# Optimization experiments

Hardware: AMD Instinct MI355X
Metric: run time of the kernel (lower is better)

## Reference

```python
import jax, jax.numpy as jnp
import numpy as np

EMBED_SIZE = 1024
HEADS = 16
HEAD_DIM = EMBED_SIZE // HEADS
N, L = 2, 2048


def setup_inputs() -> dict:
    key = jax.random.key(0)
    ks = jax.random.split(key, 6)
    values = jax.random.normal(ks[0], (N, L, EMBED_SIZE), dtype=jnp.float32)
    keys_t = jax.random.normal(ks[1], (N, L, EMBED_SIZE), dtype=jnp.float32)
    query = jax.random.normal(ks[2], (N, L, EMBED_SIZE), dtype=jnp.float32)
    mask = jax.random.randint(ks[3], (N, 1, L, L), 0, 2, dtype=jnp.int32)
    # fc_out params (torch Linear: y = x @ W.T + b)
    Wo = jax.random.normal(ks[4], (EMBED_SIZE, EMBED_SIZE), dtype=jnp.float32) * (EMBED_SIZE ** -0.5)
    bo = jax.random.normal(ks[5], (EMBED_SIZE,), dtype=jnp.float32) * 0.01
    return {"values": values, "keys": keys_t, "query": query, "mask": mask, "Wo": Wo, "bo": bo}


def reference(values, keys, query, mask, Wo, bo):
    # NOTE: the original torch module defines per-head q/k/v Linears but never
    # calls them in forward; only fc_out is applied. We reproduce that exactly.
    n, q_len, _ = query.shape
    v = values.reshape(n, -1, HEADS, HEAD_DIM)   # nkhd
    k = keys.reshape(n, -1, HEADS, HEAD_DIM)     # nkhd
    q = query.reshape(n, q_len, HEADS, HEAD_DIM) # nqhd
    energy = jnp.einsum('nqhd,nkhd->nhqk', q, k)
    energy = jnp.where(mask == 0, jnp.float32(-1e20), energy)
    scale = jnp.float32(EMBED_SIZE) ** 0.5  # sqrt(embed_size), as in source
    attn = jax.nn.softmax(energy / scale, axis=3)
    out = jnp.einsum('nhqk,nkhd->nqhd', attn, v).reshape(n, q_len, HEADS * HEAD_DIM)
    return out @ Wo.T + bo
```

## Files before the change

### kernel.cpp

```cpp
#include <hip/hip_runtime.h>
#include <hip/hip_bf16.h>
#include <stdint.h>

#define LSEQ 2048
#define NBATCH 2
#define NHEADS 16
#define HDIM 64
#define EMB 1024

typedef __bf16 bf16x8 __attribute__((ext_vector_type(8)));
typedef float f32x4 __attribute__((ext_vector_type(4)));
typedef unsigned short ushort4v __attribute__((ext_vector_type(4)));
typedef unsigned short ushort8v __attribute__((ext_vector_type(8)));

#define QSCALE (1.44269504088896f / 32.0f)

static __device__ __forceinline__ unsigned short f2bf(float f) {
  union { float f; uint32_t u; } v; v.f = f;
  uint32_t u = v.u;
  u += 0x7fffu + ((u >> 16) & 1u);
  return (unsigned short)(u >> 16);
}

static __device__ __forceinline__ f32x4 mfma16(bf16x8 a, bf16x8 b, f32x4 c) {
  return __builtin_amdgcn_mfma_f32_16x16x32_bf16(a, b, c, 0, 0, 0);
}

static __device__ __forceinline__ float mexp2(float e, uint32_t m, int b) {
  uint32_t keep = (uint32_t)__builtin_amdgcn_sbfe((int)m, b, 1);
  return __uint_as_float(__float_as_uint(__builtin_amdgcn_exp2f(e)) & keep);
}

__global__ __launch_bounds__(256) void prep_kernel(
    const float* __restrict__ q, const float* __restrict__ k,
    const float* __restrict__ w, const int* __restrict__ mask,
    const float* __restrict__ v,
    unsigned short* __restrict__ qb, unsigned short* __restrict__ kb,
    unsigned short* __restrict__ wb, unsigned char* __restrict__ mb8,
    unsigned short* __restrict__ vt) {
  int b = blockIdx.x;
  if (b < 8192) {
    int idx = b * 256 + threadIdx.x;
    const float* src; unsigned short* dst; int t; int swz;
    if (idx < (1 << 20)) { src = q; dst = qb; t = idx; swz = 0; }
    else                 { src = k; dst = kb; t = idx - (1 << 20); swz = 1; }
    int e = t << 2;
    int d = e & 63;
    int h = (e >> 6) & 15;
    int l = (e >> 10) & (LSEQ - 1);
    int n = e >> 21;
    float4 vv = reinterpret_cast<const float4*>(src)[t];
    int dd = d;
    if (swz) dd = ((((d >> 3) ^ (l & 7)) << 3) | (d & 7));
    else { vv.x *= QSCALE; vv.y *= QSCALE; vv.z *= QSCALE; vv.w *= QSCALE; }
    ushort4v o;
    o.x = f2bf(vv.x); o.y = f2bf(vv.y); o.z = f2bf(vv.z); o.w = f2bf(vv.w);
    size_t oi = (((size_t)n * NHEADS + h) * LSEQ + l) * HDIM + dd;
    *reinterpret_cast<ushort4v*>(dst + oi) = o;
  } else if (b < 9216) {
    int t = (b - 8192) * 256 + threadIdx.x;
    float4 vv = reinterpret_cast<const float4*>(w)[t];
    ushort4v o;
    o.x = f2bf(vv.x); o.y = f2bf(vv.y); o.z = f2bf(vv.z); o.w = f2bf(vv.w);
    reinterpret_cast<ushort4v*>(wb)[t] = o;
  } else if (b < 13312) {
    int idx = (b - 9216) * 256 + threadIdx.x;
    const int* mp = mask + (size_t)idx * 8;
    int4 m0 = *reinterpret_cast<const int4*>(mp);
    int4 m1 = *reinterpret_cast<const int4*>(mp + 4);
    unsigned int bb = (m0.x ? 1u : 0u) | (m0.y ? 2u : 0u) | (m0.z ? 4u : 0u) |
                      (m0.w ? 8u : 0u) | (m1.x ? 16u : 0u) | (m1.y ? 32u : 0u) |
                      (m1.z ? 64u : 0u) | (m1.w ? 128u : 0u);
    mb8[idx] = (unsigned char)bb;
  } else {
    int b2 = b - 13312;
    int kc = b2 & 63;
    int h  = (b2 >> 6) & 15;
    int n  = b2 >> 10;
    int t  = threadIdx.x;
    int d    = t & 63;
    int sgrp = t >> 6;
    const float* src = v + (size_t)n * LSEQ * EMB + h * HDIM + d;
    ushort8v o;
#pragma unroll
    for (int j = 0; j < 8; ++j) {
      int kp = (j < 4) ? (4 * sgrp + j) : (16 + 4 * sgrp + (j - 4));
      float f = src[(size_t)(kc * 32 + kp) * EMB];
      o[j] = f2bf(f);
    }
    int cs = sgrp ^ ((d >> 1) & 3);
    size_t base = (((size_t)(n * NHEADS + h) * 64 + kc) * HDIM + d) * 32 + (cs << 3);
    *reinterpret_cast<ushort8v*>(vt + base) = o;
  }
}

__global__ __launch_bounds__(256, 4) void attn_kernel(
    const unsigned short* __restrict__ Kb, const unsigned short* __restrict__ Qb,
    const unsigned short* __restrict__ VT, const uint32_t* __restrict__ maskw,
    unsigned short* __restrict__ Op) {
  __shared__ unsigned short lds[2][8192];

  int bid = blockIdx.x;
  bid = (bid & 7) * 128 + (bid >> 3);
  int qt = bid & 31;
  int h  = (bid >> 5) & 15;
  int n  = bid >> 9;
  int tid  = threadIdx.x;
  int wave = tid >> 6;
  int lane = tid & 63;
  int g  = lane >> 4;
  int qi = lane & 15;
  int qrow = qt * 64 + wave * 16 + qi;

  const unsigned short* qptr = Qb + (((size_t)n * NHEADS + h) * LSEQ + qrow) * HDIM;
  bf16x8 bq0 = *reinterpret_cast<const bf16x8*>(qptr + g * 8);
  bf16x8 bq1 = *reinterpret_cast<const bf16x8*>(qptr + 32 + g * 8);

  const unsigned short* khead  = Kb + (((size_t)n * NHEADS + h) * LSEQ) * HDIM;
  const unsigned short* vthead = VT + ((size_t)(n * NHEADS + h) * 64) * (HDIM * 32);
  const uint32_t* mrow = maskw + ((size_t)n * LSEQ + qrow) * 64;

  int xk = qi & 7;
  int kA = qi * 64 + ((g ^ xk) << 3);
  int kB = qi * 64 + (((4 + g) ^ xk) << 3);
  int kC = kA + 1024;
  int kD = kB + 1024;
  int xv = (qi >> 1) & 3;
  int vA = qi * 32 + ((g ^ xv) << 3);
  int vB = vA + 512;
  int vC = vA + 1024;
  int vD = vA + 1536;

  f32x4 z = {0.f, 0.f, 0.f, 0.f};
  f32x4 acc0 = z, acc1 = z, acc2 = z, acc3 = z;
  float ssum = 0.f;

#define STAGE(T, BUF) do {                                                     \
    const unsigned short* kg_ = khead  + (size_t)(T) * 4096 + tid * 8;         \
    const unsigned short* vg_ = vthead + (size_t)(T) * 4096 + tid * 8;         \
    __builtin_amdgcn_global_load_lds(                                          \
        (const __attribute__((address_space(1))) uint32_t*)kg_,                \
        (__attribute__((address_space(3))) uint32_t*)&lds[BUF][wave * 512],    \
        16, 0, 0);                                                             \
    __builtin_amdgcn_global_load_lds(                                          \
        (const __attribute__((address_space(1))) uint32_t*)(kg_ + 2048),       \
        (__attribute__((address_space(3))) uint32_t*)&lds[BUF][2048 + wave * 512], \
        16, 0, 0);                                                             \
    __builtin_amdgcn_global_load_lds(                                          \
        (const __attribute__((address_space(1))) uint32_t*)vg_,                \
        (__attribute__((address_space(3))) uint32_t*)&lds[BUF][4096 + wave * 512], \
        16, 0, 0);                                                             \
    __builtin_amdgcn_global_load_lds(                                          \
        (const __attribute__((address_space(1))) uint32_t*)(vg_ + 2048),       \
        (__attribute__((address_space(3))) uint32_t*)&lds[BUF][6144 + wave * 512], \
        16, 0, 0);                                                             \
  } while (0)

#define COMPUTE(BUF, CH, MW) do {                                              \
    const unsigned short* lk_ = &lds[BUF][(CH) * 2048];                        \
    const unsigned short* lv_ = &lds[BUF][4096 + (CH) * 2048];                 \
    bf16x8 K0 = *(const bf16x8*)(lk_ + kA);                                    \
    bf16x8 K1 = *(const bf16x8*)(lk_ + kB);                                    \
    bf16x8 K2 = *(const bf16x8*)(lk_ + kC);                                    \
    bf16x8 K3 = *(const bf16x8*)(lk_ + kD);                                    \
    f32x4 e0 = z, e1 = z;                                                      \
    e0 = mfma16(K0, bq0, e0); e0 = mfma16(K1, bq1, e0);                        \
    e1 = mfma16(K2, bq0, e1); e1 = mfma16(K3, bq1, e1);                        \
    uint32_t m0_ = (MW) >> (4 * g);                                            \
    uint32_t m1_ = (MW) >> (16 + 4 * g);                                       \
    float p0 = mexp2(e0[0], m0_, 0);                                           \
    float p1 = mexp2(e0[1], m0_, 1);                                           \
    float p2 = mexp2(e0[2], m0_, 2);                                           \
    float p3 = mexp2(e0[3], m0_, 3);                                           \
    float p4 = mexp2(e1[0], m1_, 0);                                           \
    float p5 = mexp2(e1[1], m1_, 1);                                           \
    float p6 = mexp2(e1[2], m1_, 2);                                           \
    float p7 = mexp2(e1[3], m1_, 3);                                           \
    ssum += ((p0 + p1) + (p2 + p3)) + ((p4 + p5) + (p6 + p7));                 \
    union { uint32_t u[4]; bf16x8 v; } pf;                                     \
    asm("v_cvt_pk_bf16_f32 %0, %1, %2" : "=v"(pf.u[0]) : "v"(p0), "v"(p1));    \
    asm("v_cvt_pk_bf16_f32 %0, %1, %2" : "=v"(pf.u[1]) : "v"(p2), "v"(p3));    \
    asm("v_cvt_pk_bf16_f32 %0, %1, %2" : "=v"(pf.u[2]) : "v"(p4), "v"(p5));    \
    asm("v_cvt_pk_bf16_f32 %0, %1, %2" : "=v"(pf.u[3]) : "v"(p6), "v"(p7));    \
    bf16x8 V0 = *(const bf16x8*)(lv_ + vA);                                    \
    bf16x8 V1 = *(const bf16x8*)(lv_ + vB);                                    \
    bf16x8 V2 = *(const bf16x8*)(lv_ + vC);                                    \
    bf16x8 V3 = *(const bf16x8*)(lv_ + vD);                                    \
    acc0 = mfma16(V0, pf.v, acc0);                                             \
    acc1 = mfma16(V1, pf.v, acc1);                                             \
    acc2 = mfma16(V2, pf.v, acc2);                                             \
    acc3 = mfma16(V3, pf.v, acc3);                                             \
  } while (0)

  uint64_t mp0 = *(const uint64_t*)(mrow);
  uint64_t mp1, mp2;
  STAGE(0, 0);
  __syncthreads();

  for (int t = 0; t < 32; t += 2) {
    int t1 = (t + 1) & 31;
    mp1 = *(const uint64_t*)(mrow + 2 * t1);
    STAGE(t1, 1);
    COMPUTE(0, 0, (uint32_t)mp0);
    COMPUTE(0, 1, (uint32_t)(mp0 >> 32));
    __syncthreads();
    int t2 = (t + 2) & 31;
    mp2 = *(const uint64_t*)(mrow + 2 * t2);
    STAGE(t2, 0);
    COMPUTE(1, 0, (uint32_t)mp1);
    COMPUTE(1, 1, (uint32_t)(mp1 >> 32));
    __syncthreads();
    mp0 = mp2;
  }
#undef STAGE
#undef COMPUTE

  ssum += __shfl_xor(ssum, 16, 64);
  ssum += __shfl_xor(ssum, 32, 64);
  float inv = 1.0f / ssum;

  size_t ob = ((size_t)n * LSEQ + qrow) * EMB + h * HDIM;
  ushort4v s0, s1, s2, s3;
#pragma unroll
  for (int r = 0; r < 4; ++r) {
    s0[r] = f2bf(acc0[r] * inv);
    s1[r] = f2bf(acc1[r] * inv);
    s2[r] = f2bf(acc2[r] * inv);
    s3[r] = f2bf(acc3[r] * inv);
  }
  *reinterpret_cast<ushort4v*>(Op + ob + 0  + 4 * g) = s0;
  *reinterpret_cast<ushort4v*>(Op + ob + 16 + 4 * g) = s1;
  *reinterpret_cast<ushort4v*>(Op + ob + 32 + 4 * g) = s2;
  *reinterpret_cast<ushort4v*>(Op + ob + 48 + 4 * g) = s3;
}

__global__ __launch_bounds__(256, 2) void proj_kernel(
    const unsigned short* __restrict__ A, const unsigned short* __restrict__ B,
    const float* __restrict__ bo, float* __restrict__ out) {
  __shared__ unsigned short plds[2][6144];

  int bid = blockIdx.x;
  bid = (bid & 7) * 64 + (bid >> 3);
  int mb0 = (bid >> 4) * 128;
  int nb0 = (bid & 15) * 64;
  int tid  = threadIdx.x;
  int wave = tid >> 6;
  int lane = tid & 63;
  int g  = lane >> 4;
  int qi = lane & 15;
  int wm = wave >> 1, wn = wave & 1;

  int srow = tid >> 2;
  int scol = (((tid & 3) ^ ((tid >> 3) & 3)) << 3);
  const unsigned short* aS0 = A + (size_t)(mb0 + srow) * EMB + scol;
  const unsigned short* aS1 = aS0 + (size_t)64 * EMB;
  const unsigned short* bS  = B + (size_t)(nb0 + srow) * EMB + scol;

  int xa = (qi >> 1) & 3;
  int gof = ((g ^ xa) << 3);
  int aof0 = (wm * 64 + qi) * 32 + gof;
  int aof1 = aof0 + 16 * 32;
  int aof2 = aof0 + 32 * 32;
  int aof3 = aof0 + 48 * 32;
  int bof0 = (wn * 32 + qi) * 32 + gof;
  int bof1 = bof0 + 16 * 32;

  f32x4 z = {0.f, 0.f, 0.f, 0.f};
  f32x4 acc00 = z, acc01 = z, acc10 = z, acc11 = z;
  f32x4 acc20 = z, acc21 = z, acc30 = z, acc31 = z;

#define PSTAGE(KT, BUF) do {                                                   \
    __builtin_amdgcn_global_load_lds(                                          \
        (const __attribute__((address_space(1))) uint32_t*)(aS0 + (KT) * 32),  \
        (__attribute__((address_space(3))) uint32_t*)&plds[BUF][wave * 512],   \
        16, 0, 0);                                                             \
    __builtin_amdgcn_global_load_lds(                                          \
        (const __attribute__((address_space(1))) uint32_t*)(aS1 + (KT) * 32),  \
        (__attribute__((address_space(3))) uint32_t*)&plds[BUF][2048 + wave * 512], \
        16, 0, 0);                                                             \
    __builtin_amdgcn_global_load_lds(                                          \
        (const __attribute__((address_space(1))) uint32_t*)(bS + (KT) * 32),   \
        (__attribute__((address_space(3))) uint32_t*)&plds[BUF][4096 + wave * 512], \
        16, 0, 0);                                                             \
  } while (0)

#define PCOMPUTE(BUF) do {                                                     \
    const unsigned short* la_ = &plds[BUF][0];                                 \
    const unsigned short* lb_ = &plds[BUF][4096];                              \
    bf16x8 a0 = *(const bf16x8*)(la_ + aof0);                                  \
    bf16x8 a1 = *(const bf16x8*)(la_ + aof1);                                  \
    bf16x8 a2 = *(const bf16x8*)(la_ + aof2);                                  \
    bf16x8 a3 = *(const bf16x8*)(la_ + aof3);                                  \
    bf16x8 b0 = *(const bf16x8*)(lb_ + bof0);                                  \
    bf16x8 b1 = *(const bf16x8*)(lb_ + bof1);                                  \
    acc00 = mfma16(a0, b0, acc00); acc01 = mfma16(a0, b1, acc01);              \
    acc10 = mfma16(a1, b0, acc10); acc11 = mfma16(a1, b1, acc11);              \
    acc20 = mfma16(a2, b0, acc20); acc21 = mfma16(a2, b1, acc21);              \
    acc30 = mfma16(a3, b0, acc30); acc31 = mfma16(a3, b1, acc31);              \
  } while (0)

  PSTAGE(0, 0);
  __syncthreads();
  for (int kt = 0; kt < 32; kt += 2) {
    PSTAGE(kt + 1, 1);
    PCOMPUTE(0);
    __syncthreads();
    PSTAGE((kt + 2) & 31, 0);
    PCOMPUTE(1);
    __syncthreads();
  }
#undef PSTAGE
#undef PCOMPUTE

  int orow = mb0 + wm * 64 + 4 * g;
  int col0 = nb0 + wn * 32 + qi;
  float bia0 = bo[col0];
  float bia1 = bo[col0 + 16];
#define PSTORE(ACC0, ACC1, M) do {                                             \
    _Pragma("unroll")                                                          \
    for (int r = 0; r < 4; ++r) {                                              \
      size_t rw = (size_t)(orow + (M) * 16 + r) * EMB;                         \
      out[rw + col0]      = ACC0[r] + bia0;                                    \
      out[rw + col0 + 16] = ACC1[r] + bia1;                                    \
    }                                                                          \
  } while (0)
  PSTORE(acc00, acc01, 0);
  PSTORE(acc10, acc11, 1);
  PSTORE(acc20, acc21, 2);
  PSTORE(acc30, acc31, 3);
#undef PSTORE
}

extern "C" void kernel_launch(void* const* d_in, const int* in_sizes, int n_in,
                              void* d_out, int out_size, void* d_ws, size_t ws_size,
                              hipStream_t stream) {
  const float* Vf   = (const float*)d_in[0];
  const float* Kf   = (const float*)d_in[1];
  const float* Qf   = (const float*)d_in[2];
  const int*   Mask = (const int*)d_in[3];
  const float* Wo   = (const float*)d_in[4];
  const float* Bo   = (const float*)d_in[5];
  float* out = (float*)d_out;

  char* ws = (char*)d_ws;
  unsigned short* Qb  = (unsigned short*)(ws);
  unsigned short* Kb  = (unsigned short*)(ws + (size_t)8  * 1024 * 1024);
  unsigned short* VTb = (unsigned short*)(ws + (size_t)16 * 1024 * 1024);
  unsigned short* Wob = (unsigned short*)(ws + (size_t)24 * 1024 * 1024);
  unsigned short* Opb = (unsigned short*)(ws + (size_t)26 * 1024 * 1024);
  unsigned char*  Mb  = (unsigned char*)(ws + (size_t)34 * 1024 * 1024);

  prep_kernel<<<15360, 256, 0, stream>>>(Qf, Kf, Wo, Mask, Vf, Qb, Kb, Wob, Mb, VTb);
  attn_kernel<<<1024, 256, 0, stream>>>(Kb, Qb, VTb, (const uint32_t*)Mb, Opb);
  proj_kernel<<<512, 256, 0, stream>>>(Opb, Wob, Bo, out);
}
```

Before: 90.59 us.

## Process two 16-row query tiles per wave to reuse K/V LDS tiles

Each attention block now covers 128 query rows instead of 64, with each wave handling two 16-row query groups that share the same K and V fragments loaded from LDS. This halves the global-to-LDS K/V staging traffic per query and the number of blocks (1024 to 512). In exchange it doubles the accumulator registers, lowers the occupancy hint to 2 blocks per CU, and 512 blocks may underfill the 256 CUs relative to before.

```diff
diff --git a/kernel.cpp b/kernel.cpp
--- a/kernel.cpp
+++ b/kernel.cpp
@@ -94,31 +94,34 @@
   }
 }
 
-__global__ __launch_bounds__(256, 4) void attn_kernel(
+__global__ __launch_bounds__(256, 2) void attn_kernel(
     const unsigned short* __restrict__ Kb, const unsigned short* __restrict__ Qb,
     const unsigned short* __restrict__ VT, const uint32_t* __restrict__ maskw,
     unsigned short* __restrict__ Op) {
   __shared__ unsigned short lds[2][8192];
 
   int bid = blockIdx.x;
-  bid = (bid & 7) * 128 + (bid >> 3);
-  int qt = bid & 31;
-  int h  = (bid >> 5) & 15;
-  int n  = bid >> 9;
+  bid = (bid & 7) * 64 + (bid >> 3);
+  int qt = bid & 15;
+  int h  = (bid >> 4) & 15;
+  int n  = bid >> 8;
   int tid  = threadIdx.x;
   int wave = tid >> 6;
   int lane = tid & 63;
   int g  = lane >> 4;
   int qi = lane & 15;
-  int qrow = qt * 64 + wave * 16 + qi;
+  int qrow = qt * 128 + wave * 16 + qi;
 
   const unsigned short* qptr = Qb + (((size_t)n * NHEADS + h) * LSEQ + qrow) * HDIM;
   bf16x8 bq0 = *reinterpret_cast<const bf16x8*>(qptr + g * 8);
   bf16x8 bq1 = *reinterpret_cast<const bf16x8*>(qptr + 32 + g * 8);
+  bf16x8 bq2 = *reinterpret_cast<const bf16x8*>(qptr + 64 * HDIM + g * 8);
+  bf16x8 bq3 = *reinterpret_cast<const bf16x8*>(qptr + 64 * HDIM + 32 + g * 8);
 
   const unsigned short* khead  = Kb + (((size_t)n * NHEADS + h) * LSEQ) * HDIM;
   const unsigned short* vthead = VT + ((size_t)(n * NHEADS + h) * 64) * (HDIM * 32);
-  const uint32_t* mrow = maskw + ((size_t)n * LSEQ + qrow) * 64;
+  const uint32_t* mrow0 = maskw + ((size_t)n * LSEQ + qrow) * 64;
+  const uint32_t* mrow1 = mrow0 + 64 * 64;
 
   int xk = qi & 7;
   int kA = qi * 64 + ((g ^ xk) << 3);
@@ -133,7 +136,8 @@
 
   f32x4 z = {0.f, 0.f, 0.f, 0.f};
   f32x4 acc0 = z, acc1 = z, acc2 = z, acc3 = z;
-  float ssum = 0.f;
+  f32x4 acc4 = z, acc5 = z, acc6 = z, acc7 = z;
+  float ssum0 = 0.f, ssum1 = 0.f;
 
 #define STAGE(T, BUF) do {                                                     \
     const unsigned short* kg_ = khead  + (size_t)(T) * 4096 + tid * 8;         \
@@ -156,82 +160,123 @@
         16, 0, 0);                                                             \
   } while (0)
 
-#define COMPUTE(BUF, CH, MW) do {                                              \
+#define COMPUTE(BUF, CH, MA, MB) do {                                          \
     const unsigned short* lk_ = &lds[BUF][(CH) * 2048];                        \
     const unsigned short* lv_ = &lds[BUF][4096 + (CH) * 2048];                 \
     bf16x8 K0 = *(const bf16x8*)(lk_ + kA);                                    \
     bf16x8 K1 = *(const bf16x8*)(lk_ + kB);                                    \
     bf16x8 K2 = *(const bf16x8*)(lk_ + kC);                                    \
     bf16x8 K3 = *(const bf16x8*)(lk_ + kD);                                    \
-    f32x4 e0 = z, e1 = z;                                                      \
+    f32x4 e0 = z, e1 = z, f0 = z, f1 = z;                                      \
     e0 = mfma16(K0, bq0, e0); e0 = mfma16(K1, bq1, e0);                        \
     e1 = mfma16(K2, bq0, e1); e1 = mfma16(K3, bq1, e1);                        \
-    uint32_t m0_ = (MW) >> (4 * g);                                            \
-    uint32_t m1_ = (MW) >> (16 + 4 * g);                                       \
-    float p0 = mexp2(e0[0], m0_, 0);                                           \
-    float p1 = mexp2(e0[1], m0_, 1);                                           \
-    float p2 = mexp2(e0[2], m0_, 2);                                           \
-    float p3 = mexp2(e0[3], m0_, 3);                                           \
-    float p4 = mexp2(e1[0], m1_, 0);                                           \
-    float p5 = mexp2(e1[1], m1_, 1);                                           \
-    float p6 = mexp2(e1[2], m1_, 2);                                           \
-    float p7 = mexp2(e1[3], m1_, 3);                                           \
-    ssum += ((p0 + p1) + (p2 + p3)) + ((p4 + p5) + (p6 + p7));                 \
-    union { uint32_t u[4]; bf16x8 v; } pf;                                     \
-    asm("v_cvt_pk_bf16_f32 %0, %1, %2" : "=v"(pf.u[0]) : "v"(p0), "v"(p1));    \
-    asm("v_cvt_pk_bf16_f32 %0, %1, %2" : "=v"(pf.u[1]) : "v"(p2), "v"(p3));    \
-    asm("v_cvt_pk_bf16_f32 %0, %1, %2" : "=v"(pf.u[2]) : "v"(p4), "v"(p5));    \
-    asm("v_cvt_pk_bf16_f32 %0, %1, %2" : "=v"(pf.u[3]) : "v"(p6), "v"(p7));    \
+    f0 = mfma16(K0, bq2, f0); f0 = mfma16(K1, bq3, f0);                        \
+    f1 = mfma16(K2, bq2, f1); f1 = mfma16(K3, bq3, f1);                        \
     bf16x8 V0 = *(const bf16x8*)(lv_ + vA);                                    \
     bf16x8 V1 = *(const bf16x8*)(lv_ + vB);                                    \
     bf16x8 V2 = *(const bf16x8*)(lv_ + vC);                                    \
     bf16x8 V3 = *(const bf16x8*)(lv_ + vD);                                    \
-    acc0 = mfma16(V0, pf.v, acc0);                                             \
-    acc1 = mfma16(V1, pf.v, acc1);                                             \
-    acc2 = mfma16(V2, pf.v, acc2);                                             \
-    acc3 = mfma16(V3, pf.v, acc3);                                             \
+    {                                                                          \
+      uint32_t m0_ = (MA) >> (4 * g);                                          \
+      uint32_t m1_ = (MA) >> (16 + 4 * g);                                     \
+      float p0 = mexp2(e0[0], m0_, 0);                                         \
+      float p1 = mexp2(e0[1], m0_, 1);                                         \
+      float p2 = mexp2(e0[2], m0_, 2);                                         \
+      float p3 = mexp2(e0[3], m0_, 3);                                         \
+      float p4 = mexp2(e1[0], m1_, 0);                                         \
+      float p5 = mexp2(e1[1], m1_, 1);                                         \
+      float p6 = mexp2(e1[2], m1_, 2);                                         \
+      float p7 = mexp2(e1[3], m1_, 3);                                         \
+      ssum0 += ((p0 + p1) + (p2 + p3)) + ((p4 + p5) + (p6 + p7));              \
+      union { uint32_t u[4]; bf16x8 v; } pf;                                   \
+      asm("v_cvt_pk_bf16_f32 %0, %1, %2" : "=v"(pf.u[0]) : "v"(p0), "v"(p1));  \
+      asm("v_cvt_pk_bf16_f32 %0, %1, %2" : "=v"(pf.u[1]) : "v"(p2), "v"(p3));  \
+      asm("v_cvt_pk_bf16_f32 %0, %1, %2" : "=v"(pf.u[2]) : "v"(p4), "v"(p5));  \
+      asm("v_cvt_pk_bf16_f32 %0, %1, %2" : "=v"(pf.u[3]) : "v"(p6), "v"(p7));  \
+      acc0 = mfma16(V0, pf.v, acc0);                                           \
+      acc1 = mfma16(V1, pf.v, acc1);                                           \
+      acc2 = mfma16(V2, pf.v, acc2);                                           \
+      acc3 = mfma16(V3, pf.v, acc3);                                           \
+    }                                                                          \
+    {                                                                          \
+      uint32_t m0_ = (MB) >> (4 * g);                                          \
+      uint32_t m1_ = (MB) >> (16 + 4 * g);                                     \
+      float r0 = mexp2(f0[0], m0_, 0);                                         \
+      float r1 = mexp2(f0[1], m0_, 1);                                         \
+      float r2 = mexp2(f0[2], m0_, 2);                                         \
+      float r3 = mexp2(f0[3], m0_, 3);                                         \
+      float r4 = mexp2(f1[0], m1_, 0);                                         \
+      float r5 = mexp2(f1[1], m1_, 1);                                         \
+      float r6 = mexp2(f1[2], m1_, 2);                                         \
+      float r7 = mexp2(f1[3], m1_, 3);                                         \
+      ssum1 += ((r0 + r1) + (r2 + r3)) + ((r4 + r5) + (r6 + r7));              \
+      union { uint32_t u[4]; bf16x8 v; } pg;                                   \
+      asm("v_cvt_pk_bf16_f32 %0, %1, %2" : "=v"(pg.u[0]) : "v"(r0), "v"(r1));  \
+      asm("v_cvt_pk_bf16_f32 %0, %1, %2" : "=v"(pg.u[1]) : "v"(r2), "v"(r3));  \
+      asm("v_cvt_pk_bf16_f32 %0, %1, %2" : "=v"(pg.u[2]) : "v"(r4), "v"(r5));  \
+      asm("v_cvt_pk_bf16_f32 %0, %1, %2" : "=v"(pg.u[3]) : "v"(r6), "v"(r7));  \
+      acc4 = mfma16(V0, pg.v, acc4);                                           \
+      acc5 = mfma16(V1, pg.v, acc5);                                           \
+      acc6 = mfma16(V2, pg.v, acc6);                                           \
+      acc7 = mfma16(V3, pg.v, acc7);                                           \
+    }                                                                          \
   } while (0)
 
-  uint64_t mp0 = *(const uint64_t*)(mrow);
-  uint64_t mp1, mp2;
+  uint64_t ma0 = *(const uint64_t*)(mrow0);
+  uint64_t mb0 = *(const uint64_t*)(mrow1);
+  uint64_t ma1, mb1, ma2, mb2;
   STAGE(0, 0);
   __syncthreads();
 
   for (int t = 0; t < 32; t += 2) {
     int t1 = (t + 1) & 31;
-    mp1 = *(const uint64_t*)(mrow + 2 * t1);
+    ma1 = *(const uint64_t*)(mrow0 + 2 * t1);
+    mb1 = *(const uint64_t*)(mrow1 + 2 * t1);
     STAGE(t1, 1);
-    COMPUTE(0, 0, (uint32_t)mp0);
-    COMPUTE(0, 1, (uint32_t)(mp0 >> 32));
+    COMPUTE(0, 0, (uint32_t)ma0, (uint32_t)mb0);
+    COMPUTE(0, 1, (uint32_t)(ma0 >> 32), (uint32_t)(mb0 >> 32));
     __syncthreads();
     int t2 = (t + 2) & 31;
-    mp2 = *(const uint64_t*)(mrow + 2 * t2);
+    ma2 = *(const uint64_t*)(mrow0 + 2 * t2);
+    mb2 = *(const uint64_t*)(mrow1 + 2 * t2);
     STAGE(t2, 0);
-    COMPUTE(1, 0, (uint32_t)mp1);
-    COMPUTE(1, 1, (uint32_t)(mp1 >> 32));
+    COMPUTE(1, 0, (uint32_t)ma1, (uint32_t)mb1);
+    COMPUTE(1, 1, (uint32_t)(ma1 >> 32), (uint32_t)(mb1 >> 32));
     __syncthreads();
-    mp0 = mp2;
+    ma0 = ma2; mb0 = mb2;
   }
 #undef STAGE
 #undef COMPUTE
 
-  ssum += __shfl_xor(ssum, 16, 64);
-  ssum += __shfl_xor(ssum, 32, 64);
-  float inv = 1.0f / ssum;
-
-  size_t ob = ((size_t)n * LSEQ + qrow) * EMB + h * HDIM;
-  ushort4v s0, s1, s2, s3;
+  ssum0 += __shfl_xor(ssum0, 16, 64);
+  ssum0 += __shfl_xor(ssum0, 32, 64);
+  ssum1 += __shfl_xor(ssum1, 16, 64);
+  ssum1 += __shfl_xor(ssum1, 32, 64);
+  float inv0 = 1.0f / ssum0;
+  float inv1 = 1.0f / ssum1;
+
+  size_t ob0 = ((size_t)n * LSEQ + qrow) * EMB + h * HDIM;
+  size_t ob1 = ob0 + (size_t)64 * EMB;
+  ushort4v s0, s1, s2, s3, s4, s5, s6, s7;
 #pragma unroll
   for (int r = 0; r < 4; ++r) {
-    s0[r] = f2bf(acc0[r] * inv);
-    s1[r] = f2bf(acc1[r] * inv);
-    s2[r] = f2bf(acc2[r] * inv);
-    s3[r] = f2bf(acc3[r] * inv);
+    s0[r] = f2bf(acc0[r] * inv0);
+    s1[r] = f2bf(acc1[r] * inv0);
+    s2[r] = f2bf(acc2[r] * inv0);
+    s3[r] = f2bf(acc3[r] * inv0);
+    s4[r] = f2bf(acc4[r] * inv1);
+    s5[r] = f2bf(acc5[r] * inv1);
+    s6[r] = f2bf(acc6[r] * inv1);
+    s7[r] = f2bf(acc7[r] * inv1);
   }
-  *reinterpret_cast<ushort4v*>(Op + ob + 0  + 4 * g) = s0;
-  *reinterpret_cast<ushort4v*>(Op + ob + 16 + 4 * g) = s1;
-  *reinterpret_cast<ushort4v*>(Op + ob + 32 + 4 * g) = s2;
-  *reinterpret_cast<ushort4v*>(Op + ob + 48 + 4 * g) = s3;
+  *reinterpret_cast<ushort4v*>(Op + ob0 + 0  + 4 * g) = s0;
+  *reinterpret_cast<ushort4v*>(Op + ob0 + 16 + 4 * g) = s1;
+  *reinterpret_cast<ushort4v*>(Op + ob0 + 32 + 4 * g) = s2;
+  *reinterpret_cast<ushort4v*>(Op + ob0 + 48 + 4 * g) = s3;
+  *reinterpret_cast<ushort4v*>(Op + ob1 + 0  + 4 * g) = s4;
+  *reinterpret_cast<ushort4v*>(Op + ob1 + 16 + 4 * g) = s5;
+  *reinterpret_cast<ushort4v*>(Op + ob1 + 32 + 4 * g) = s6;
+  *reinterpret_cast<ushort4v*>(Op + ob1 + 48 + 4 * g) = s7;
 }
 
 __global__ __launch_bounds__(256, 2) void proj_kernel(
@@ -351,6 +396,6 @@
   unsigned char*  Mb  = (unsigned char*)(ws + (size_t)34 * 1024 * 1024);
 
   prep_kernel<<<15360, 256, 0, stream>>>(Qf, Kf, Wo, Mask, Vf, Qb, Kb, Wob, Mb, VTb);
-  attn_kernel<<<1024, 256, 0, stream>>>(Kb, Qb, VTb, (const uint32_t*)Mb, Opb);
+  attn_kernel<<<512, 256, 0, stream>>>(Kb, Qb, VTb, (const uint32_t*)Mb, Opb);
   proj_kernel<<<512, 256, 0, stream>>>(Opb, Wob, Bo, out);
 }
```

After: 89.48 us. Within noise of the previous version (-1.2%).

## Stream K-only tiles through LDS, read V directly from global, MFMA row sums

Applied to the files above, without the earlier changes.

Only K tiles are staged in LDS now, each stage covering 128 keys instead of 64, with four compute chunks per stage. V fragments are read straight from global memory (L2/L1) in fragment-ready layout, so the V swizzle is dropped. The softmax denominator is accumulated with an extra MFMA against a ones vector instead of scalar adds and cross-lane shuffles. This halves the LDS/barrier count per key but puts V global-load latency on the critical path of each chunk.

```diff
diff --git a/kernel.cpp b/kernel.cpp
--- a/kernel.cpp
+++ b/kernel.cpp
@@ -88,8 +88,7 @@
       float f = src[(size_t)(kc * 32 + kp) * EMB];
       o[j] = f2bf(f);
     }
-    int cs = sgrp ^ ((d >> 1) & 3);
-    size_t base = (((size_t)(n * NHEADS + h) * 64 + kc) * HDIM + d) * 32 + (cs << 3);
+    size_t base = (((size_t)(n * NHEADS + h) * 64 + kc) * HDIM + d) * 32 + (sgrp << 3);
     *reinterpret_cast<ushort8v*>(vt + base) = o;
   }
 }
@@ -125,40 +124,31 @@
   int kB = qi * 64 + (((4 + g) ^ xk) << 3);
   int kC = kA + 1024;
   int kD = kB + 1024;
-  int xv = (qi >> 1) & 3;
-  int vA = qi * 32 + ((g ^ xv) << 3);
-  int vB = vA + 512;
-  int vC = vA + 1024;
-  int vD = vA + 1536;
+  int vA = qi * 32 + g * 8;
+
+  union { uint32_t u[4]; bf16x8 v; } ones;
+  ones.u[0] = 0x3F803F80u; ones.u[1] = 0x3F803F80u;
+  ones.u[2] = 0x3F803F80u; ones.u[3] = 0x3F803F80u;
 
   f32x4 z = {0.f, 0.f, 0.f, 0.f};
   f32x4 acc0 = z, acc1 = z, acc2 = z, acc3 = z;
-  float ssum = 0.f;
+  f32x4 sacc = z;
 
 #define STAGE(T, BUF) do {                                                     \
-    const unsigned short* kg_ = khead  + (size_t)(T) * 4096 + tid * 8;         \
-    const unsigned short* vg_ = vthead + (size_t)(T) * 4096 + tid * 8;         \
-    __builtin_amdgcn_global_load_lds(                                          \
-        (const __attribute__((address_space(1))) uint32_t*)kg_,                \
-        (__attribute__((address_space(3))) uint32_t*)&lds[BUF][wave * 512],    \
-        16, 0, 0);                                                             \
-    __builtin_amdgcn_global_load_lds(                                          \
-        (const __attribute__((address_space(1))) uint32_t*)(kg_ + 2048),       \
-        (__attribute__((address_space(3))) uint32_t*)&lds[BUF][2048 + wave * 512], \
-        16, 0, 0);                                                             \
-    __builtin_amdgcn_global_load_lds(                                          \
-        (const __attribute__((address_space(1))) uint32_t*)vg_,                \
-        (__attribute__((address_space(3))) uint32_t*)&lds[BUF][4096 + wave * 512], \
-        16, 0, 0);                                                             \
-    __builtin_amdgcn_global_load_lds(                                          \
-        (const __attribute__((address_space(1))) uint32_t*)(vg_ + 2048),       \
-        (__attribute__((address_space(3))) uint32_t*)&lds[BUF][6144 + wave * 512], \
-        16, 0, 0);                                                             \
-  } while (0)
-
-#define COMPUTE(BUF, CH, MW) do {                                              \
+    const unsigned short* kg_ = khead + (size_t)(T) * 8192 + tid * 8;          \
+    _Pragma("unroll")                                                          \
+    for (int j_ = 0; j_ < 4; ++j_) {                                           \
+      __builtin_amdgcn_global_load_lds(                                        \
+          (const __attribute__((address_space(1))) uint32_t*)(kg_ + j_ * 2048),\
+          (__attribute__((address_space(3))) uint32_t*)                        \
+              &lds[BUF][j_ * 2048 + wave * 512],                               \
+          16, 0, 0);                                                           \
+    }                                                                          \
+  } while (0)
+
+#define COMPUTE(BUF, CH, KC, MW) do {                                          \
     const unsigned short* lk_ = &lds[BUF][(CH) * 2048];                        \
-    const unsigned short* lv_ = &lds[BUF][4096 + (CH) * 2048];                 \
+    const unsigned short* vc_ = vthead + (size_t)(KC) * 2048;                  \
     bf16x8 K0 = *(const bf16x8*)(lk_ + kA);                                    \
     bf16x8 K1 = *(const bf16x8*)(lk_ + kB);                                    \
     bf16x8 K2 = *(const bf16x8*)(lk_ + kC);                                    \
@@ -166,6 +156,10 @@
     f32x4 e0 = z, e1 = z;                                                      \
     e0 = mfma16(K0, bq0, e0); e0 = mfma16(K1, bq1, e0);                        \
     e1 = mfma16(K2, bq0, e1); e1 = mfma16(K3, bq1, e1);                        \
+    bf16x8 V0 = *(const bf16x8*)(vc_ + vA);                                    \
+    bf16x8 V1 = *(const bf16x8*)(vc_ + vA + 512);                              \
+    bf16x8 V2 = *(const bf16x8*)(vc_ + vA + 1024);                             \
+    bf16x8 V3 = *(const bf16x8*)(vc_ + vA + 1536);                             \
     uint32_t m0_ = (MW) >> (4 * g);                                            \
     uint32_t m1_ = (MW) >> (16 + 4 * g);                                       \
     float p0 = mexp2(e0[0], m0_, 0);                                           \
@@ -176,48 +170,46 @@
     float p5 = mexp2(e1[1], m1_, 1);                                           \
     float p6 = mexp2(e1[2], m1_, 2);                                           \
     float p7 = mexp2(e1[3], m1_, 3);                                           \
-    ssum += ((p0 + p1) + (p2 + p3)) + ((p4 + p5) + (p6 + p7));                 \
     union { uint32_t u[4]; bf16x8 v; } pf;                                     \
     asm("v_cvt_pk_bf16_f32 %0, %1, %2" : "=v"(pf.u[0]) : "v"(p0), "v"(p1));    \
     asm("v_cvt_pk_bf16_f32 %0, %1, %2" : "=v"(pf.u[1]) : "v"(p2), "v"(p3));    \
     asm("v_cvt_pk_bf16_f32 %0, %1, %2" : "=v"(pf.u[2]) : "v"(p4), "v"(p5));    \
     asm("v_cvt_pk_bf16_f32 %0, %1, %2" : "=v"(pf.u[3]) : "v"(p6), "v"(p7));    \
-    bf16x8 V0 = *(const bf16x8*)(lv_ + vA);                                    \
-    bf16x8 V1 = *(const bf16x8*)(lv_ + vB);                                    \
-    bf16x8 V2 = *(const bf16x8*)(lv_ + vC);                                    \
-    bf16x8 V3 = *(const bf16x8*)(lv_ + vD);                                    \
     acc0 = mfma16(V0, pf.v, acc0);                                             \
     acc1 = mfma16(V1, pf.v, acc1);                                             \
     acc2 = mfma16(V2, pf.v, acc2);                                             \
     acc3 = mfma16(V3, pf.v, acc3);                                             \
-  } while (0)
-
-  uint64_t mp0 = *(const uint64_t*)(mrow);
-  uint64_t mp1, mp2;
+    sacc = mfma16(ones.v, pf.v, sacc);                                         \
+  } while (0)
+
+  uint4 mw0 = *(const uint4*)(mrow);
+  uint4 mw1, mw2;
   STAGE(0, 0);
   __syncthreads();
 
-  for (int t = 0; t < 32; t += 2) {
-    int t1 = (t + 1) & 31;
-    mp1 = *(const uint64_t*)(mrow + 2 * t1);
+  for (int t = 0; t < 16; t += 2) {
+    int t1 = (t + 1) & 15;
+    mw1 = *(const uint4*)(mrow + 4 * t1);
     STAGE(t1, 1);
-    COMPUTE(0, 0, (uint32_t)mp0);
-    COMPUTE(0, 1, (uint32_t)(mp0 >> 32));
+    COMPUTE(0, 0, t * 4 + 0, mw0.x);
+    COMPUTE(0, 1, t * 4 + 1, mw0.y);
+    COMPUTE(0, 2, t * 4 + 2, mw0.z);
+    COMPUTE(0, 3, t * 4 + 3, mw0.w);
     __syncthreads();
-    int t2 = (t + 2) & 31;
-    mp2 = *(const uint64_t*)(mrow + 2 * t2);
+    int t2 = (t + 2) & 15;
+    mw2 = *(const uint4*)(mrow + 4 * t2);
     STAGE(t2, 0);
-    COMPUTE(1, 0, (uint32_t)mp1);
-    COMPUTE(1, 1, (uint32_t)(mp1 >> 32));
+    COMPUTE(1, 0, t1 * 4 + 0, mw1.x);
+    COMPUTE(1, 1, t1 * 4 + 1, mw1.y);
+    COMPUTE(1, 2, t1 * 4 + 2, mw1.z);
+    COMPUTE(1, 3, t1 * 4 + 3, mw1.w);
     __syncthreads();
-    mp0 = mp2;
+    mw0 = mw2;
   }
 #undef STAGE
 #undef COMPUTE
 
-  ssum += __shfl_xor(ssum, 16, 64);
-  ssum += __shfl_xor(ssum, 32, 64);
-  float inv = 1.0f / ssum;
+  float inv = 1.0f / sacc[0];
 
   size_t ob = ((size_t)n * LSEQ + qrow) * EMB + h * HDIM;
   ushort4v s0, s1, s2, s3;
```

After: 116.8 us. +28.9%, slower.
